# Optimization experiments

Hardware: AMD Instinct MI355X
Metric: run time of the kernel (lower is better)

Reference implementation:

```python
import jax, jax.numpy as jnp
import numpy as np

N_NODES = 50000
N_EDGES = 800000
C_IN = 64
C_OUT = 64
K = 3


def setup_inputs() -> dict:
    key = jax.random.key(0)
    k1, k2, k3, k4, k5, k6 = jax.random.split(key, 6)
    x = jax.random.normal(k1, (N_NODES, C_IN), dtype=jnp.float32)
    edge_index = jax.random.randint(k2, (2, N_EDGES), 0, N_NODES, dtype=jnp.int32)
    edge_weight = jax.random.uniform(k3, (N_EDGES,), dtype=jnp.float32)
    # Xavier-uniform init for [K, C_IN, C_OUT] (fan over last two dims)
    limit = float(np.sqrt(6.0 / (C_IN + C_OUT)))
    theta_forward = jax.random.uniform(k4, (K, C_IN, C_OUT), minval=-limit, maxval=limit, dtype=jnp.float32)
    theta_backward = jax.random.uniform(k5, (K, C_IN, C_OUT), minval=-limit, maxval=limit, dtype=jnp.float32)
    return {
        "x": x,
        "edge_index": edge_index,
        "edge_weight": edge_weight,
        "theta_forward": theta_forward,
        "theta_backward": theta_backward,
    }


def _propagate(x, row, col, edge_weight, n_nodes):
    # degree normalization: deg[i] = sum of edge_weight over edges with row == i
    deg = jax.ops.segment_sum(edge_weight, row, num_segments=n_nodes)
    deg_inv = jnp.where(deg > 0, jax.lax.rsqrt(jnp.where(deg > 0, deg, 1.0)), 0.0)
    norm = deg_inv[row] * edge_weight * deg_inv[col]      # [E]
    msg = norm[:, None] * x[col]                          # [E, C] gather-scale
    return jax.ops.segment_sum(msg, row, num_segments=n_nodes)  # scatter-add -> [N, C]


def reference(x, edge_index, edge_weight, theta_forward, theta_backward):
    row, col = edge_index[0], edge_index[1]
    n_nodes = x.shape[0]
    k = theta_forward.shape[0]
    Tx_0 = x
    Tx_1 = _propagate(x, row, col, edge_weight, n_nodes)
    out = Tx_0 @ theta_forward[0] + Tx_1 @ theta_backward[0]
    for i in range(1, k):
        Tx_2 = _propagate(Tx_1, row, col, edge_weight, n_nodes)
        out = out + Tx_2 @ theta_forward[i] + Tx_1 @ theta_backward[i]
        Tx_1 = Tx_2
    return out
```

## Files before the change

### kernel.cpp

```cpp
#include <hip/hip_runtime.h>
#include <hip/hip_fp16.h>


#define N_NODES 50000
#define N_EDGES 800000
#define C 64
#define CAP 64
#define NPART 196
#define CAPP 4608
#define EPB 8192
#define NEB 98
#define XH_BLOCKS 782
#define CW_BLOCKS 16

typedef _Float16 half8 __attribute__((ext_vector_type(8)));
typedef float f32x4 __attribute__((ext_vector_type(4)));

__global__ __launch_bounds__(1024) void scatter2_kernel(
        const int* __restrict__ row, const int* __restrict__ col,
        const float* __restrict__ w, int* __restrict__ percur,
        uint2* __restrict__ pedges,
        const float* __restrict__ x, __half* __restrict__ xh,
        const float* __restrict__ tf, const float* __restrict__ tb,
        _Float16* __restrict__ whc) {
    const int tid = threadIdx.x;
    if (blockIdx.x >= NEB + XH_BLOCKS) {
        int idx = (blockIdx.x - NEB - XH_BLOCKS) * 1024 + tid;
        int j = idx >> 12;
        int rem = idx & 4095;
        int ci = rem >> 6;
        int co = rem & 63;
        float v;
        if (j == 0)      v = tf[rem];
        else if (j == 1) v = tb[rem] + tb[4096 + rem];
        else if (j == 2) v = tf[4096 + rem] + tb[8192 + rem];
        else             v = tf[8192 + rem];
        whc[(j << 12) + (co << 6) + ci] = (_Float16)v;
        return;
    }
    if (blockIdx.x >= NEB) {
        int i = (blockIdx.x - NEB) * 1024 + tid;
        if (i < N_NODES * C / 4) {
            float4 v = ((const float4*)x)[i];
            union { float2 f2; __half2 h2[2]; } u;
            u.h2[0] = __floats2half2_rn(v.x, v.y);
            u.h2[1] = __floats2half2_rn(v.z, v.w);
            ((float2*)xh)[i] = u.f2;
        }
        return;
    }
    __shared__ int h[NPART];
    __shared__ int cur[NPART];
    uint2 ent[8];
    int pp[8];
    if (tid < NPART) h[tid] = 0;
    __syncthreads();
    int base = blockIdx.x * EPB;
#pragma unroll
    for (int i = 0; i < 8; ++i) {
        int e = base + i * 1024 + tid;
        pp[i] = -1;
        if (e < N_EDGES) {
            int r = row[e];
            unsigned int c = (unsigned int)col[e];
            unsigned int wh = (unsigned int)__half_as_ushort(__float2half_rn(w[e]));
            ent[i] = make_uint2((c << 16) | wh, (unsigned int)(r & 255));
            pp[i] = r >> 8;
            atomicAdd(&h[pp[i]], 1);
        }
    }
    __syncthreads();
    if (tid < NPART) cur[tid] = atomicAdd(&percur[tid], h[tid]);
    __syncthreads();
#pragma unroll
    for (int i = 0; i < 8; ++i) {
        if (pp[i] >= 0) {
            int slot = atomicAdd(&cur[pp[i]], 1);
            pedges[(size_t)pp[i] * CAPP + slot] = ent[i];
        }
    }
}

__global__ __launch_bounds__(1024) void build_kernel(
        const uint2* __restrict__ pedges, const int* __restrict__ percur,
        unsigned int* __restrict__ bkt, int* __restrict__ cnt,
        float* __restrict__ dinv) {
    __shared__ unsigned int lbuck[256 * CAP];
    __shared__ int lcnt[256];
    const int tid = threadIdx.x;
    const int p = blockIdx.x;
    if (tid < 256) lcnt[tid] = 0;
    __syncthreads();
    int e = min(percur[p], CAPP);
    const uint2* src = pedges + (size_t)p * CAPP;
    for (int i = tid; i < e; i += 1024) {
        uint2 en = src[i];
        int rl = (int)en.y;
        int slot = atomicAdd(&lcnt[rl], 1);
        if (slot < CAP) lbuck[(rl << 6) + slot] = en.x;
    }
    __syncthreads();
    if (tid < 256) {
        int m = min(lcnt[tid], CAP);
        int g = (p << 8) + tid;
        float sum = 0.f;
        for (int j = 0; j < m; ++j)
            sum += __half2float(__ushort_as_half(
                (unsigned short)(lbuck[(tid << 6) + j] & 0xFFFFu)));
        if (g < N_NODES) {
            cnt[g] = m;
            dinv[g] = (sum > 0.f) ? rsqrtf(sum) : 0.f;
        }
    }
    __syncthreads();
    {
        int r = tid >> 2;
        int ch = tid & 3;
        int m = min(lcnt[r], CAP);
        const uint4* s4 = (const uint4*)&lbuck[r << 6];
        uint4* dst = (uint4*)(bkt + (((size_t)(p << 8) + r) << 6));
        for (int j = ch; (j << 2) < m; j += 4) dst[j] = s4[j];
    }
}

template <bool FIXW, bool FUSE_GEMM>
__global__ __launch_bounds__(256) void prop_kernel(
        const __half* __restrict__ xin, __half* __restrict__ xout,
        const int* __restrict__ cnt, unsigned int* __restrict__ bkt,
        const float* __restrict__ dinv,
        const __half* __restrict__ x0, const __half* __restrict__ x1,
        const _Float16* __restrict__ whc, float* __restrict__ out) {
    const int tid = threadIdx.x;
    const int wib = tid >> 6;
    const int lane = tid & 63;
    const int q = lane >> 4;
    const int ql = lane & 15;
    const int node = (blockIdx.x << 4) + (wib << 2) + q;
    int m = min(cnt[node], CAP);
    int base = node << 6;
    int cj[4];
    float nj[4];
#pragma unroll
    for (int s = 0; s < 4; ++s) {
        int idx = (s << 4) + ql;
        cj[s] = 0;
        nj[s] = 0.f;
        if (idx < m) {
            unsigned int b = bkt[base + idx];
            int c = (int)(b >> 16);
            cj[s] = c << 6;
            float wv = __half2float(__ushort_as_half((unsigned short)(b & 0xFFFFu)));
            if constexpr (FIXW) {
                float nn = wv * dinv[c];
                nj[s] = nn;
                bkt[base + idx] = ((unsigned int)c << 16) |
                    (unsigned int)__half_as_ushort(__float2half_rn(nn));
            } else {
                nj[s] = wv;
            }
        }
    }
    float ax = 0.f, ay = 0.f, az = 0.f, aw = 0.f;
#pragma unroll
    for (int s = 0; s < 4; ++s) {
        int cb = s << 4;
        if (cb >= m) break;
        int rem = m - cb;
        if (rem > 16) rem = 16;
        int mm = (rem + 7) & ~7;
        for (int jo = 0; jo < mm; jo += 8) {
            int cs[8];
            float ns[8];
            float2 vs[8];
#pragma unroll
            for (int t = 0; t < 8; ++t) {
                cs[t] = __shfl(cj[s], (q << 4) + jo + t);
                ns[t] = __shfl(nj[s], (q << 4) + jo + t);
            }
#pragma unroll
            for (int t = 0; t < 8; ++t)
                vs[t] = *(const float2*)(xin + cs[t] + (ql << 2));
#pragma unroll
            for (int t = 0; t < 8; ++t) {
                const __half2* hp = (const __half2*)&vs[t];
                float2 a = __half22float2(hp[0]);
                float2 b = __half22float2(hp[1]);
                ax += ns[t] * a.x;
                ay += ns[t] * a.y;
                az += ns[t] * b.x;
                aw += ns[t] * b.y;
            }
        }
    }
    float dr = dinv[node];
    union { float2 f2; __half2 h2[2]; } u;
    u.h2[0] = __floats2half2_rn(dr * ax, dr * ay);
    u.h2[1] = __floats2half2_rn(dr * az, dr * aw);
    if constexpr (!FUSE_GEMM) {
        *(float2*)(xout + ((size_t)node << 6) + (ql << 2)) = u.f2;
    } else {
        __shared__ _Float16 tcl[16 * 72];
        *(float2*)(void*)&tcl[((wib << 2) + q) * 72 + (ql << 2)] = u.f2;
        __syncthreads();
        const int mbase = blockIdx.x << 4;
        const __half* gsrc[3] = {x0, x1, xin};
        const size_t abase = ((size_t)(mbase + ql) << 6) + (q << 3);
        f32x4 acc = {};
#pragma unroll
        for (int j = 0; j < 4; ++j) {
#pragma unroll
            for (int kk = 0; kk < 64; kk += 32) {
                half8 af;
                if (j < 3)
                    af = *(const half8*)(const void*)(gsrc[j] + abase + kk);
                else
                    af = *(const half8*)(const void*)&tcl[ql * 72 + (q << 3) + kk];
                const _Float16* wb = whc + (j << 12) + (((wib << 4) + ql) << 6)
                                         + (q << 3) + kk;
                half8 bf = *(const half8*)(const void*)wb;
                acc = __builtin_amdgcn_mfma_f32_16x16x32_f16(af, bf, acc, 0, 0, 0);
            }
        }
#pragma unroll
        for (int i = 0; i < 4; ++i) {
            int r = mbase + (q << 2) + i;
            out[((size_t)r << 6) + (wib << 4) + ql] = acc[i];
        }
    }
}

extern "C" void kernel_launch(void* const* d_in, const int* in_sizes, int n_in,
                              void* d_out, int out_size, void* d_ws, size_t ws_size,
                              hipStream_t stream) {
    const float* x  = (const float*)d_in[0];
    const int*   ei = (const int*)d_in[1];
    const float* ew = (const float*)d_in[2];
    const float* tf = (const float*)d_in[3];
    const float* tb = (const float*)d_in[4];
    float* out = (float*)d_out;

    const int* row = ei;
    const int* col = ei + N_EDGES;

    const int NROWS_PAD = NPART * 256;
    float* ws = (float*)d_ws;
    size_t off = 0;
    int*    percur = (int*)(ws + off); off += 256;
    uint2*  pedges = (uint2*)(ws + off); off += (size_t)NPART * CAPP * 2;
    unsigned int* bkt = (unsigned int*)(ws + off); off += (size_t)NROWS_PAD * CAP;
    int*    cnt  = (int*)(ws + off); off += NROWS_PAD;
    float*  dinv = ws + off; off += NROWS_PAD;
    __half* xh   = (__half*)(ws + off); off += (size_t)N_NODES * C / 2;
    __half* tA   = (__half*)(ws + off); off += (size_t)N_NODES * C / 2;
    __half* tB   = (__half*)(ws + off); off += (size_t)N_NODES * C / 2;
    __half* tC   = (__half*)(ws + off); off += (size_t)N_NODES * C / 2;
    _Float16* whc = (_Float16*)(ws + off); off += 4 * 64 * 64 / 2;

    hipMemsetAsync(percur, 0, NPART * sizeof(int), stream);

    scatter2_kernel<<<NEB + XH_BLOCKS + CW_BLOCKS, 1024, 0, stream>>>(
        row, col, ew, percur, pedges, x, xh, tf, tb, whc);
    build_kernel<<<NPART, 1024, 0, stream>>>(pedges, percur, bkt, cnt, dinv);

    const int PB = N_NODES / 16;
    prop_kernel<true,  false><<<PB, 256, 0, stream>>>(
        xh, tA, cnt, bkt, dinv, nullptr, nullptr, nullptr, nullptr);
    prop_kernel<false, false><<<PB, 256, 0, stream>>>(
        tA, tB, cnt, bkt, dinv, nullptr, nullptr, nullptr, nullptr);
    prop_kernel<false, true><<<PB, 256, 0, stream>>>(
        tB, tC, cnt, bkt, dinv, xh, tA, whc, out);
}
```

Measured before the change: 158.9 us.

## Remap propagation to one wavefront per node with 16-byte gathers

Each node is now processed by a full 64-lane wavefront. Eight groups of 8 lanes each gather a 128-byte half8 row, so up to 8 edges are loaded in flight per group, and the partial sums are combined with cross-lane xor shuffles. Before, four nodes shared a wave and each lane gathered 8 bytes per edge. The change aims to widen memory transactions and raise memory-level parallelism for the irregular gathers. The cost is more reduction shuffles and idle lanes for nodes of low degree. The final fused-GEMM launch uses 1024-thread blocks of 16 nodes, with only the first 256 threads doing the MFMA, and the unused tC buffer is dropped.

```diff
diff --git a/kernel.cpp b/kernel.cpp
--- a/kernel.cpp
+++ b/kernel.cpp
@@ -123,89 +123,82 @@
     }
 }
 
-template <bool FIXW, bool FUSE_GEMM>
-__global__ __launch_bounds__(256) void prop_kernel(
+template <bool FIRST, bool FUSE_GEMM, int NPB>
+__global__ __launch_bounds__(NPB * 64) void prop_kernel(
         const __half* __restrict__ xin, __half* __restrict__ xout,
         const int* __restrict__ cnt, unsigned int* __restrict__ bkt,
         const float* __restrict__ dinv,
         const __half* __restrict__ x0, const __half* __restrict__ x1,
         const _Float16* __restrict__ whc, float* __restrict__ out) {
+    __shared__ _Float16 tcl[16 * 72];
     const int tid = threadIdx.x;
     const int wib = tid >> 6;
     const int lane = tid & 63;
-    const int q = lane >> 4;
-    const int ql = lane & 15;
-    const int node = (blockIdx.x << 4) + (wib << 2) + q;
-    int m = min(cnt[node], CAP);
-    int base = node << 6;
-    int cj[4];
-    float nj[4];
-#pragma unroll
-    for (int s = 0; s < 4; ++s) {
-        int idx = (s << 4) + ql;
-        cj[s] = 0;
-        nj[s] = 0.f;
-        if (idx < m) {
-            unsigned int b = bkt[base + idx];
-            int c = (int)(b >> 16);
-            cj[s] = c << 6;
-            float wv = __half2float(__ushort_as_half((unsigned short)(b & 0xFFFFu)));
-            if constexpr (FIXW) {
-                float nn = wv * dinv[c];
-                nj[s] = nn;
-                bkt[base + idx] = ((unsigned int)c << 16) |
-                    (unsigned int)__half_as_ushort(__float2half_rn(nn));
-            } else {
-                nj[s] = wv;
-            }
-        }
-    }
-    float ax = 0.f, ay = 0.f, az = 0.f, aw = 0.f;
-#pragma unroll
-    for (int s = 0; s < 4; ++s) {
-        int cb = s << 4;
-        if (cb >= m) break;
-        int rem = m - cb;
-        if (rem > 16) rem = 16;
-        int mm = (rem + 7) & ~7;
-        for (int jo = 0; jo < mm; jo += 8) {
-            int cs[8];
-            float ns[8];
-            float2 vs[8];
-#pragma unroll
-            for (int t = 0; t < 8; ++t) {
-                cs[t] = __shfl(cj[s], (q << 4) + jo + t);
-                ns[t] = __shfl(nj[s], (q << 4) + jo + t);
-            }
-#pragma unroll
-            for (int t = 0; t < 8; ++t)
-                vs[t] = *(const float2*)(xin + cs[t] + (ql << 2));
-#pragma unroll
-            for (int t = 0; t < 8; ++t) {
-                const __half2* hp = (const __half2*)&vs[t];
-                float2 a = __half22float2(hp[0]);
-                float2 b = __half22float2(hp[1]);
-                ax += ns[t] * a.x;
-                ay += ns[t] * a.y;
-                az += ns[t] * b.x;
-                aw += ns[t] * b.y;
-            }
-        }
-    }
-    float dr = dinv[node];
-    union { float2 f2; __half2 h2[2]; } u;
-    u.h2[0] = __floats2half2_rn(dr * ax, dr * ay);
-    u.h2[1] = __floats2half2_rn(dr * az, dr * aw);
-    if constexpr (!FUSE_GEMM) {
-        *(float2*)(xout + ((size_t)node << 6) + (ql << 2)) = u.f2;
-    } else {
-        __shared__ _Float16 tcl[16 * 72];
-        *(float2*)(void*)&tcl[((wib << 2) + q) * 72 + (ql << 2)] = u.f2;
+    const int oct = lane >> 3;
+    const int k = lane & 7;
+    const int node = blockIdx.x * NPB + wib;
+    const int m = min(cnt[node], CAP);
+    const int base = node << 6;
+    int cl = 0;
+    float nl = 0.f;
+    if (lane < m) {
+        unsigned int b = bkt[base + lane];
+        int c = (int)(b >> 16);
+        float wv = __half2float(__ushort_as_half((unsigned short)(b & 0xFFFFu)));
+        if constexpr (FIRST) {
+            wv *= dinv[c];
+            bkt[base + lane] = ((unsigned int)c << 16) |
+                (unsigned int)__half_as_ushort(__float2half_rn(wv));
+        }
+        cl = c << 6;
+        nl = wv;
+    }
+    const int nr = (m + 7) >> 3;
+#define LOADR(r) \
+    float nn##r = 0.f; half8 v##r = {}; \
+    if (nr > r) { \
+        int cc = __shfl(cl, (r << 3) + oct); \
+        nn##r = __shfl(nl, (r << 3) + oct); \
+        v##r = *(const half8*)(const void*)(xin + cc + (k << 3)); \
+    }
+    LOADR(0) LOADR(1) LOADR(2) LOADR(3) LOADR(4) LOADR(5) LOADR(6) LOADR(7)
+#undef LOADR
+    float acc[8] = {0.f, 0.f, 0.f, 0.f, 0.f, 0.f, 0.f, 0.f};
+#define FMAR(r) \
+    if (nr > r) { \
+        _Pragma("unroll") \
+        for (int j = 0; j < 8; ++j) acc[j] += nn##r * (float)v##r[j]; \
+    }
+    FMAR(0) FMAR(1) FMAR(2) FMAR(3) FMAR(4) FMAR(5) FMAR(6) FMAR(7)
+#undef FMAR
+#pragma unroll
+    for (int j = 0; j < 8; ++j) {
+        acc[j] += __shfl_xor(acc[j], 8);
+        acc[j] += __shfl_xor(acc[j], 16);
+        acc[j] += __shfl_xor(acc[j], 32);
+    }
+    const float dr = dinv[node];
+    if (oct == 0) {
+        half8 o;
+#pragma unroll
+        for (int j = 0; j < 8; ++j) o[j] = (_Float16)(dr * acc[j]);
+        if constexpr (!FUSE_GEMM) {
+            *(half8*)(void*)(xout + ((size_t)node << 6) + (k << 3)) = o;
+        } else {
+            *(half8*)(void*)&tcl[wib * 72 + (k << 3)] = o;
+        }
+    }
+    if constexpr (FUSE_GEMM) {
         __syncthreads();
+        if (tid >= 256) return;
+        const int wv4 = tid >> 6;
+        const int lane4 = tid & 63;
+        const int quad = lane4 >> 4;
+        const int l16 = lane4 & 15;
         const int mbase = blockIdx.x << 4;
         const __half* gsrc[3] = {x0, x1, xin};
-        const size_t abase = ((size_t)(mbase + ql) << 6) + (q << 3);
-        f32x4 acc = {};
+        const size_t abase = ((size_t)(mbase + l16) << 6) + (quad << 3);
+        f32x4 acc2 = {};
 #pragma unroll
         for (int j = 0; j < 4; ++j) {
 #pragma unroll
@@ -214,17 +207,17 @@
                 if (j < 3)
                     af = *(const half8*)(const void*)(gsrc[j] + abase + kk);
                 else
-                    af = *(const half8*)(const void*)&tcl[ql * 72 + (q << 3) + kk];
-                const _Float16* wb = whc + (j << 12) + (((wib << 4) + ql) << 6)
-                                         + (q << 3) + kk;
+                    af = *(const half8*)(const void*)&tcl[l16 * 72 + (quad << 3) + kk];
+                const _Float16* wb = whc + (j << 12) + (((wv4 << 4) + l16) << 6)
+                                         + (quad << 3) + kk;
                 half8 bf = *(const half8*)(const void*)wb;
-                acc = __builtin_amdgcn_mfma_f32_16x16x32_f16(af, bf, acc, 0, 0, 0);
+                acc2 = __builtin_amdgcn_mfma_f32_16x16x32_f16(af, bf, acc2, 0, 0, 0);
             }
         }
 #pragma unroll
         for (int i = 0; i < 4; ++i) {
-            int r = mbase + (q << 2) + i;
-            out[((size_t)r << 6) + (wib << 4) + ql] = acc[i];
+            int r = mbase + (quad << 2) + i;
+            out[((size_t)r << 6) + (wv4 << 4) + l16] = acc2[i];
         }
     }
 }
@@ -253,20 +246,18 @@
     __half* xh   = (__half*)(ws + off); off += (size_t)N_NODES * C / 2;
     __half* tA   = (__half*)(ws + off); off += (size_t)N_NODES * C / 2;
     __half* tB   = (__half*)(ws + off); off += (size_t)N_NODES * C / 2;
-    __half* tC   = (__half*)(ws + off); off += (size_t)N_NODES * C / 2;
     _Float16* whc = (_Float16*)(ws + off); off += 4 * 64 * 64 / 2;
 
-    hipMemsetAsync(percur, 0, NPART * sizeof(int), stream);
+    hipMemsetAsync(percur, 0, 256 * sizeof(int), stream);
 
     scatter2_kernel<<<NEB + XH_BLOCKS + CW_BLOCKS, 1024, 0, stream>>>(
         row, col, ew, percur, pedges, x, xh, tf, tb, whc);
     build_kernel<<<NPART, 1024, 0, stream>>>(pedges, percur, bkt, cnt, dinv);
 
-    const int PB = N_NODES / 16;
-    prop_kernel<true,  false><<<PB, 256, 0, stream>>>(
+    prop_kernel<true,  false, 4><<<12500, 256, 0, stream>>>(
         xh, tA, cnt, bkt, dinv, nullptr, nullptr, nullptr, nullptr);
-    prop_kernel<false, false><<<PB, 256, 0, stream>>>(
+    prop_kernel<false, false, 4><<<12500, 256, 0, stream>>>(
         tA, tB, cnt, bkt, dinv, nullptr, nullptr, nullptr, nullptr);
-    prop_kernel<false, true><<<PB, 256, 0, stream>>>(
-        tB, tC, cnt, bkt, dinv, xh, tA, whc, out);
-}
+    prop_kernel<false, true, 16><<<3125, 1024, 0, stream>>>(
+        tB, nullptr, cnt, bkt, dinv, xh, tA, whc, out);
+}
```

Result: slower. 174.2 us (+9.6%).
